# Kernel optimization log

Hardware: AMD Instinct MI355X
Metric: run time of the kernel (lower is better)

Reference implementation:

```python
import jax, jax.numpy as jnp
import numpy as np

S, B, I, H = 512, 64, 512, 512
KEEP = 0.75  # 1 - dropout_p, p = 0.25


def _mask(key, shape):
    # inverted-dropout mask, sampled once per sequence (variational dropout)
    return (jax.random.uniform(key, shape) < KEEP).astype(jnp.float32) / KEEP


def setup_inputs() -> dict:
    key = jax.random.key(0)
    ks = jax.random.split(key, 10)
    s_i0 = 1.0 / np.sqrt(I)
    s_i1 = 1.0 / np.sqrt(2 * H)
    s_h = 1.0 / np.sqrt(H)
    return {
        "x": jax.random.normal(ks[0], (S, B, I), jnp.float32),
        "W_ih_l0": jax.random.normal(ks[1], (2, 4 * H, I), jnp.float32) * s_i0,
        "W_ih_l1": jax.random.normal(ks[2], (2, 4 * H, 2 * H), jnp.float32) * s_i1,
        "W_hh": jax.random.normal(ks[3], (4, 4 * H, H), jnp.float32) * s_h,
        "b_ih": jax.random.normal(ks[4], (4, 4 * H), jnp.float32) * s_h,
        "b_hh": jax.random.normal(ks[5], (4, 4 * H), jnp.float32) * s_h,
        "mask_x0": _mask(ks[6], (2, B, I)),
        "mask_x1": _mask(ks[7], (2, B, 2 * H)),
        "mask_h": _mask(ks[8], (4, B, H)),
    }


def _run_cell(x, W_ih, W_hh, b_ih, b_hh, mx, mh, reverse):
    # x: [S, B, in]; returns out [S, B, H], (h_n, c_n) each [B, H]
    xs = x[::-1] if reverse else x
    # precompute input projections for all timesteps (one big GEMM)
    xp = jnp.einsum('sbi,gi->sbg', xs * mx, W_ih) + b_ih  # [S, B, 4H]
    h = W_hh.shape[1]
    h0 = jnp.zeros((x.shape[1], h), x.dtype)

    def step(carry, xp_t):
        hh, cc = carry
        gates = xp_t + (hh * mh) @ W_hh.T + b_hh  # variational hidden dropout
        gi, gf, gg, go = jnp.split(gates, 4, axis=-1)  # torch LSTMCell order i,f,g,o
        cc = jax.nn.sigmoid(gf) * cc + jax.nn.sigmoid(gi) * jnp.tanh(gg)
        hh = jax.nn.sigmoid(go) * jnp.tanh(cc)
        return (hh, cc), hh

    (hn, cn), out = jax.lax.scan(step, (h0, h0), xp)
    out = out[::-1] if reverse else out
    return out, hn, cn


def reference(x, W_ih_l0, W_ih_l1, W_hh, b_ih, b_hh, mask_x0, mask_x1, mask_h):
    W_ih = [W_ih_l0, W_ih_l1]
    mask_x = [mask_x0, mask_x1]
    inp = x
    h_list, c_list = [], []
    for layer in range(2):
        outs = []
        for d in range(2):  # 0: forward, 1: backward
            idx = 2 * layer + d
            o, hn, cn = _run_cell(inp, W_ih[layer][d], W_hh[idx], b_ih[idx],
                                  b_hh[idx], mask_x[layer][d], mask_h[idx],
                                  reverse=(d == 1))
            outs.append(o)
            h_list.append(hn)
            c_list.append(cn)
        inp = jnp.concatenate(outs, axis=-1)  # [S, B, 2H]
    return inp, jnp.stack(h_list, 0), jnp.stack(c_list, 0)
```

## Files before the change

### kernel.cpp

```cpp
#include <hip/hip_runtime.h>
#include <math.h>


typedef float f32x4 __attribute__((ext_vector_type(4)));

#define SLEN   512
#define HID    512
#define CHK    64
#define APAD   68
#define OUT_SEQ  (SLEN*64*2*HID)
#define STATE_SZ (4*64*HID)

__global__ __launch_bounds__(256) void init_ws(float* __restrict__ hmT,
                                               unsigned* __restrict__ bar) {
    const int b = blockIdx.x, t = threadIdx.x;
    if (b < 128) {
        *(f32x4*)(hmT + (b*256 + t)*4) = (f32x4){0.f, 0.f, 0.f, 0.f};
    } else {
        bar[(b - 128)*256 + t] = 0u;
    }
}

__device__ __forceinline__ void bar_arrive(unsigned* bar, int g) {
    __syncthreads();
    if (threadIdx.x == 0) {
        unsigned lo = __hip_atomic_fetch_add(bar + (g & 31)*16, 1u,
                          __ATOMIC_RELAXED, __HIP_MEMORY_SCOPE_AGENT);
        if (lo == 7u) {
            unsigned ro = __hip_atomic_fetch_add(bar + 512, 1u,
                              __ATOMIC_RELAXED, __HIP_MEMORY_SCOPE_AGENT);
            if (ro == 31u) {
                for (int i = 0; i < 32; ++i)
                    __hip_atomic_store(bar + i*16, 0u,
                        __ATOMIC_RELAXED, __HIP_MEMORY_SCOPE_AGENT);
                __hip_atomic_store(bar + 512, 0u,
                    __ATOMIC_RELAXED, __HIP_MEMORY_SCOPE_AGENT);
                asm volatile("s_waitcnt vmcnt(0)" ::: "memory");
                __hip_atomic_fetch_add(bar + 513, 1u,
                    __ATOMIC_RELAXED, __HIP_MEMORY_SCOPE_AGENT);
            }
        }
    }
}

__device__ __forceinline__ void bar_wait(unsigned* bar, unsigned s) {
    if (threadIdx.x == 0) {
        while (__hip_atomic_load(bar + 513, __ATOMIC_RELAXED,
                                 __HIP_MEMORY_SCOPE_AGENT) < s)
            __builtin_amdgcn_s_sleep(1);
    }
    __syncthreads();
}

template<int LAYER>
__global__ __launch_bounds__(256) void lstm_layer(
    const float* __restrict__ x,
    const float* __restrict__ Wih0,
    const float* __restrict__ Wih1,
    const float* __restrict__ Whh,
    const float* __restrict__ bih,
    const float* __restrict__ bhh,
    const float* __restrict__ mx0,
    const float* __restrict__ mx1,
    const float* __restrict__ mhm,
    float* __restrict__ out0,
    float* __restrict__ hmT,
    unsigned* __restrict__ barbase,
    float* __restrict__ dout)
{
    constexpr int Kin = LAYER ? 1024 : 512;
    constexpr int NCH = (Kin + HID)/CHK;
    constexpr int HCH = Kin/CHK;

    __shared__ __align__(16) float At[2][CHK*APAD];
    __shared__ __align__(16) float Wt[2][CHK*16];

    unsigned* bar  = barbase + LAYER*1024;

    const int g    = blockIdx.x;
    const int dir  = g >> 7;
    const int wg   = g & 127;
    const int cell = LAYER*2 + dir;
    const int u0   = wg*4;
    const int tid  = threadIdx.x;
    const int lane = tid & 63;
    const int wv   = tid >> 6;

    const int r0 = (lane & 15)*4;
    const int c0 = (lane >> 4)*4;

    const int sb = tid >> 2;
    const int ak = (tid & 3)*4;
    const int hr = tid >> 4;
    const int hb = (tid & 15)*4;
    const int wc   = tid >> 4;
    const int wko  = (tid & 15)*4;
    const int wkey = ((tid & 15) >> 1) & 3;
    const int wpc  = (((wc >> 2) ^ wkey) << 2) | (wc & 3);
    const int gcw  = (wc >> 2)*512 + u0 + (wc & 3);

    const int pbA = (((c0 >> 2) ^ ((wv*2    ) & 3)) << 2);
    const int pbB = (((c0 >> 2) ^ ((wv*2 + 1) & 3)) << 2);

    const int eb = tid & 63;
    const int eu = tid >> 6;
    const size_t sidx = ((size_t)(cell*64 + eb))*512 + u0 + eu;
    const float bsum[4] = {
        bih[cell*2048 + 0*512 + u0 + eu] + bhh[cell*2048 + 0*512 + u0 + eu],
        bih[cell*2048 + 1*512 + u0 + eu] + bhh[cell*2048 + 1*512 + u0 + eu],
        bih[cell*2048 + 2*512 + u0 + eu] + bhh[cell*2048 + 2*512 + u0 + eu],
        bih[cell*2048 + 3*512 + u0 + eu] + bhh[cell*2048 + 3*512 + u0 + eu] };
    const float mreg = mhm[sidx];
    float* const haddr0 = hmT + ((size_t)(cell*512 + u0 + eu))*64 + eb;
    float creg = 0.0f;

    for (int s = 0; s < SLEN; ++s) {
        const int t = dir ? (SLEN-1-s) : s;
        const float* hrd = hmT + (size_t)(s & 1)*STATE_SZ;
        float* const hwr = haddr0 + (size_t)((s + 1) & 1)*STATE_SZ;

        float acc[4][4];
#pragma unroll
        for (int i = 0; i < 4; ++i)
#pragma unroll
            for (int j = 0; j < 4; ++j) acc[i][j] = 0.0f;

        f32x4 va0, va1, va2, va3, vm0, vm1, vm2, vm3, w4;
        bool xpart = true;

        auto prefetch = [&](int ch) {
            const int k0 = ch*CHK;
            xpart = (k0 < Kin);
            if (xpart) {
                const float *asrc, *amsk, *wsrc;
                if (LAYER == 0) {
                    asrc = x   + ((size_t)(t*64   + sb))*512  + k0 + ak;
                    amsk = mx0 + ((size_t)(dir*64 + sb))*512  + k0 + ak;
                    wsrc = Wih0 + (size_t)dir*2048*512  + (size_t)gcw*512  + k0 + wko;
                } else {
                    asrc = out0 + ((size_t)(t*64   + sb))*1024 + k0 + ak;
                    amsk = mx1  + ((size_t)(dir*64 + sb))*1024 + k0 + ak;
                    wsrc = Wih1 + (size_t)dir*2048*1024 + (size_t)gcw*1024 + k0 + wko;
                }
                va0 = *(const f32x4*)(asrc);      vm0 = *(const f32x4*)(amsk);
                va1 = *(const f32x4*)(asrc + 16); vm1 = *(const f32x4*)(amsk + 16);
                va2 = *(const f32x4*)(asrc + 32); vm2 = *(const f32x4*)(amsk + 32);
                va3 = *(const f32x4*)(asrc + 48); vm3 = *(const f32x4*)(amsk + 48);
                w4  = *(const f32x4*)(wsrc);
            } else {
                const int kh = k0 - Kin;
                const float* hsrc = hrd + ((size_t)(cell*512 + kh + hr))*64 + hb;
                asm volatile("global_load_dwordx4 %0, %1, off sc0 sc1 nt"
                             : "=v"(va0) : "v"(hsrc)         : "memory");
                asm volatile("global_load_dwordx4 %0, %1, off sc0 sc1 nt"
                             : "=v"(va1) : "v"(hsrc + 16*64) : "memory");
                asm volatile("global_load_dwordx4 %0, %1, off sc0 sc1 nt"
                             : "=v"(va2) : "v"(hsrc + 32*64) : "memory");
                asm volatile("global_load_dwordx4 %0, %1, off sc0 sc1 nt"
                             : "=v"(va3) : "v"(hsrc + 48*64) : "memory");
                w4  = *(const f32x4*)(Whh + (size_t)cell*2048*512
                                           + (size_t)gcw*512 + kh + wko);
            }
        };

        auto writeb = [&](float* Ab, float* Wb) {
            if (xpart) {
#define WRQ(Q, V, M)  { \
                Ab[(ak + (Q)*16 + 0)*APAD + sb] = V.x*M.x; \
                Ab[(ak + (Q)*16 + 1)*APAD + sb] = V.y*M.y; \
                Ab[(ak + (Q)*16 + 2)*APAD + sb] = V.z*M.z; \
                Ab[(ak + (Q)*16 + 3)*APAD + sb] = V.w*M.w; }
                WRQ(0, va0, vm0) WRQ(1, va1, vm1) WRQ(2, va2, vm2) WRQ(3, va3, vm3)
#undef WRQ
            } else {
                asm volatile("s_waitcnt vmcnt(0)" ::: "memory");
                *(f32x4*)(Ab + (hr +  0)*APAD + hb) = va0;
                *(f32x4*)(Ab + (hr + 16)*APAD + hb) = va1;
                *(f32x4*)(Ab + (hr + 32)*APAD + hb) = va2;
                *(f32x4*)(Ab + (hr + 48)*APAD + hb) = va3;
            }
            Wb[(wko+0)*16 + wpc] = w4.x;
            Wb[(wko+1)*16 + wpc] = w4.y;
            Wb[(wko+2)*16 + wpc] = w4.z;
            Wb[(wko+3)*16 + wpc] = w4.w;
        };

        auto compute = [&](const float* Ab, const float* Wb) {
#pragma unroll
            for (int kk = 0; kk < 16; ++kk) {
                const int krow = wv*16 + kk;
                const f32x4 a = *(const f32x4*)(Ab + krow*APAD + r0);
                const f32x4 w = *(const f32x4*)(Wb + krow*16 + (kk < 8 ? pbA : pbB));
                acc[0][0] += a.x*w.x; acc[0][1] += a.x*w.y; acc[0][2] += a.x*w.z; acc[0][3] += a.x*w.w;
                acc[1][0] += a.y*w.x; acc[1][1] += a.y*w.y; acc[1][2] += a.y*w.z; acc[1][3] += a.y*w.w;
                acc[2][0] += a.z*w.x; acc[2][1] += a.z*w.y; acc[2][2] += a.z*w.z; acc[2][3] += a.z*w.w;
                acc[3][0] += a.w*w.x; acc[3][1] += a.w*w.y; acc[3][2] += a.w*w.z; acc[3][3] += a.w*w.w;
            }
        };

        prefetch(0);
        writeb(At[0], Wt[0]);
        for (int ch = 0; ch < NCH; ++ch) {
            __syncthreads();
            if (ch == HCH - 1 && s > 0)
                bar_wait(bar, (unsigned)s);
            const int p = ch & 1;
            if (ch + 1 < NCH) prefetch(ch + 1);
            compute(At[p], Wt[p]);
            if (ch + 1 < NCH) writeb(At[p^1], Wt[p^1]);
        }

        float* red = At[0];
#pragma unroll
        for (int j = 0; j < 4; ++j) {
            f32x4 v = {acc[0][j], acc[1][j], acc[2][j], acc[3][j]};
            *(f32x4*)(red + wv*1024 + (c0+j)*64 + r0) = v;
        }
        __syncthreads();

        {
            float gq[4];
#pragma unroll
            for (int q = 0; q < 4; ++q) {
                const int c = q*4 + eu;
                gq[q] = red[c*64 + eb] + red[1024 + c*64 + eb]
                      + red[2048 + c*64 + eb] + red[3072 + c*64 + eb] + bsum[q];
            }
            const float ig = 1.0f/(1.0f + expf(-gq[0]));
            const float fg = 1.0f/(1.0f + expf(-gq[1]));
            const float gg = tanhf(gq[2]);
            const float og = 1.0f/(1.0f + expf(-gq[3]));
            const float cnew = fg*creg + ig*gg;
            const float hnew = og*tanhf(cnew);
            creg = cnew;
            const float hm = hnew * mreg;
            asm volatile("global_store_dword %0, %1, off sc0 sc1 nt"
                         :: "v"(hwr), "v"(hm) : "memory");
            float* obase = LAYER ? dout : out0;
            obase[((size_t)(t*64 + eb))*1024 + dir*512 + u0 + eu] = hnew;
            if (s == SLEN-1) {
                dout[OUT_SEQ + sidx]            = hnew;
                dout[OUT_SEQ + STATE_SZ + sidx] = cnew;
            }
        }

        if (s + 1 < SLEN) bar_arrive(bar, g);
    }
}

extern "C" void kernel_launch(void* const* d_in, const int* in_sizes, int n_in,
                              void* d_out, int out_size, void* d_ws, size_t ws_size,
                              hipStream_t stream)
{
    const float* x    = (const float*)d_in[0];
    const float* Wih0 = (const float*)d_in[1];
    const float* Wih1 = (const float*)d_in[2];
    const float* Whh  = (const float*)d_in[3];
    const float* bih  = (const float*)d_in[4];
    const float* bhh  = (const float*)d_in[5];
    const float* mx0  = (const float*)d_in[6];
    const float* mx1  = (const float*)d_in[7];
    const float* mhm  = (const float*)d_in[8];

    float* out  = (float*)d_out;
    float* out0 = (float*)d_ws;
    float* hmT  = out0 + OUT_SEQ;
    unsigned* bar = (unsigned*)(hmT + 2*STATE_SZ);

    init_ws<<<136, 256, 0, stream>>>(hmT, bar);
    lstm_layer<0><<<256, 256, 0, stream>>>(x, Wih0, Wih1, Whh, bih, bhh,
                                           mx0, mx1, mhm, out0, hmT, bar, out);
    lstm_layer<1><<<256, 256, 0, stream>>>(x, Wih0, Wih1, Whh, bih, bhh,
                                           mx0, mx1, mhm, out0, hmT, bar, out);
}
```

Before: 29.07 ms.

## Pre-transpose weights to K-major layout and read them directly from global in 512-thread blocks

Adds a kernel that transposes the input and recurrent weights into one K-major buffer, so each block reads its weight columns as coalesced vector loads instead of staging them through shared memory. The recurrent kernel moves to 512 threads with 8 waves, each wave taking a half-K slice and computing 8 gate columns, and the two halves are combined with a cross-lane shuffle before the shared-memory reduction. This removes the weight LDS staging and its swizzle, and doubles the waves per block to hide latency. The cost is an extra transpose pass over all weights on every call and heavier per-step global/L2 weight traffic.

```diff
diff --git a/kernel.cpp b/kernel.cpp
--- a/kernel.cpp
+++ b/kernel.cpp
@@ -10,6 +10,7 @@
 #define APAD   68
 #define OUT_SEQ  (SLEN*64*2*HID)
 #define STATE_SZ (4*64*HID)
+#define WT_ROWS  5120
 
 __global__ __launch_bounds__(256) void init_ws(float* __restrict__ hmT,
                                                unsigned* __restrict__ bar) {
@@ -18,6 +19,50 @@
         *(f32x4*)(hmT + (b*256 + t)*4) = (f32x4){0.f, 0.f, 0.f, 0.f};
     } else {
         bar[(b - 128)*256 + t] = 0u;
+    }
+}
+
+__global__ __launch_bounds__(256) void transpose_w(
+    const float* __restrict__ Wih0,
+    const float* __restrict__ Wih1,
+    const float* __restrict__ Whh,
+    float* __restrict__ WT)
+{
+    int id = blockIdx.x;
+    int cell, rem;
+    if (id < 1024) { cell = id >> 9;            rem = id & 511; }
+    else { id -= 1024; cell = 2 + (id >= 768);  rem = id % 768; }
+    const int ktile = rem >> 5, gtile = rem & 31;
+    const int k0 = ktile*64, g0 = gtile*64;
+    const int Kin = (cell < 2) ? 512 : 1024;
+
+    const float* src; int ks; size_t srow;
+    if (k0 < Kin) {
+        src = (cell < 2) ? Wih0 + (size_t)cell*2048*512
+                         : Wih1 + (size_t)(cell-2)*2048*1024;
+        ks = k0; srow = Kin;
+    } else {
+        src = Whh + (size_t)cell*2048*512;
+        ks = k0 - Kin; srow = 512;
+    }
+
+    __shared__ float T[64][65];
+    const int tid = threadIdx.x;
+    {
+        const int i = tid >> 2, j0 = (tid & 3)*16;
+        const float* p = src + (size_t)(g0 + i)*srow + ks + j0;
+#pragma unroll
+        for (int q = 0; q < 4; ++q)
+            *(f32x4*)(&T[i][j0 + q*4]) = *(const f32x4*)(p + q*4);
+    }
+    __syncthreads();
+    {
+        const size_t rowOff = (cell == 0) ? 0 : (cell == 1) ? 1024
+                            : (cell == 2) ? 2048 : 3584;
+        const int jj0 = (tid >> 6)*16, ii = tid & 63;
+#pragma unroll
+        for (int jj = 0; jj < 16; ++jj)
+            WT[(rowOff + k0 + jj0 + jj)*2048 + g0 + ii] = T[ii][jj0 + jj];
     }
 }
 
@@ -53,11 +98,9 @@
 }
 
 template<int LAYER>
-__global__ __launch_bounds__(256) void lstm_layer(
+__global__ __launch_bounds__(512, 2) void lstm_layer(
     const float* __restrict__ x,
-    const float* __restrict__ Wih0,
-    const float* __restrict__ Wih1,
-    const float* __restrict__ Whh,
+    const float* __restrict__ WT,
     const float* __restrict__ bih,
     const float* __restrict__ bhh,
     const float* __restrict__ mx0,
@@ -73,9 +116,8 @@
     constexpr int HCH = Kin/CHK;
 
     __shared__ __align__(16) float At[2][CHK*APAD];
-    __shared__ __align__(16) float Wt[2][CHK*16];
-
-    unsigned* bar  = barbase + LAYER*1024;
+
+    unsigned* bar = barbase + LAYER*1024;
 
     const int g    = blockIdx.x;
     const int dir  = g >> 7;
@@ -86,32 +128,35 @@
     const int lane = tid & 63;
     const int wv   = tid >> 6;
 
-    const int r0 = (lane & 15)*4;
-    const int c0 = (lane >> 4)*4;
-
-    const int sb = tid >> 2;
-    const int ak = (tid & 3)*4;
-    const int hr = tid >> 4;
-    const int hb = (tid & 15)*4;
-    const int wc   = tid >> 4;
-    const int wko  = (tid & 15)*4;
-    const int wkey = ((tid & 15) >> 1) & 3;
-    const int wpc  = (((wc >> 2) ^ wkey) << 2) | (wc & 3);
-    const int gcw  = (wc >> 2)*512 + u0 + (wc & 3);
-
-    const int pbA = (((c0 >> 2) ^ ((wv*2    ) & 3)) << 2);
-    const int pbB = (((c0 >> 2) ^ ((wv*2 + 1) & 3)) << 2);
+    const int r0    = (lane & 15)*4;
+    const int cq    = (lane >> 4) & 1;
+    const int c0    = cq*8;
+    const int kbase = wv*8 + (lane >> 5)*4;
+    const int wcb   = cq*1024 + u0;
+    const size_t rowOff = LAYER ? (2048 + (size_t)dir*1536) : ((size_t)dir*1024);
+    const float* WTc = WT + rowOff*2048;
+
+    const int sb  = tid & 63;
+    const int aks = (tid >> 6)*8;
+    const int hkrow = tid >> 3;
+    const int hb    = (tid & 7)*8;
 
     const int eb = tid & 63;
     const int eu = tid >> 6;
-    const size_t sidx = ((size_t)(cell*64 + eb))*512 + u0 + eu;
-    const float bsum[4] = {
-        bih[cell*2048 + 0*512 + u0 + eu] + bhh[cell*2048 + 0*512 + u0 + eu],
-        bih[cell*2048 + 1*512 + u0 + eu] + bhh[cell*2048 + 1*512 + u0 + eu],
-        bih[cell*2048 + 2*512 + u0 + eu] + bhh[cell*2048 + 2*512 + u0 + eu],
-        bih[cell*2048 + 3*512 + u0 + eu] + bhh[cell*2048 + 3*512 + u0 + eu] };
-    const float mreg = mhm[sidx];
-    float* const haddr0 = hmT + ((size_t)(cell*512 + u0 + eu))*64 + eb;
+    float bsum[4] = {0.f, 0.f, 0.f, 0.f};
+    float mreg = 0.f;
+    float* haddr0 = nullptr;
+    size_t sidx = 0;
+    if (tid < 256) {
+#pragma unroll
+        for (int q = 0; q < 4; ++q) {
+            const int gc = cell*2048 + q*512 + u0 + eu;
+            bsum[q] = bih[gc] + bhh[gc];
+        }
+        sidx  = ((size_t)(cell*64 + eb))*512 + u0 + eu;
+        mreg  = mhm[sidx];
+        haddr0 = hmT + ((size_t)(cell*512 + u0 + eu))*64 + eb;
+    }
     float creg = 0.0f;
 
     for (int s = 0; s < SLEN; ++s) {
@@ -119,112 +164,108 @@
         const float* hrd = hmT + (size_t)(s & 1)*STATE_SZ;
         float* const hwr = haddr0 + (size_t)((s + 1) & 1)*STATE_SZ;
 
-        float acc[4][4];
+        float acc[4][8];
 #pragma unroll
         for (int i = 0; i < 4; ++i)
 #pragma unroll
-            for (int j = 0; j < 4; ++j) acc[i][j] = 0.0f;
-
-        f32x4 va0, va1, va2, va3, vm0, vm1, vm2, vm3, w4;
+            for (int j = 0; j < 8; ++j) acc[i][j] = 0.0f;
+
+        f32x4 va0, va1, vm0, vm1;
         bool xpart = true;
 
         auto prefetch = [&](int ch) {
             const int k0 = ch*CHK;
             xpart = (k0 < Kin);
             if (xpart) {
-                const float *asrc, *amsk, *wsrc;
+                const float *asrc, *amsk;
                 if (LAYER == 0) {
-                    asrc = x   + ((size_t)(t*64   + sb))*512  + k0 + ak;
-                    amsk = mx0 + ((size_t)(dir*64 + sb))*512  + k0 + ak;
-                    wsrc = Wih0 + (size_t)dir*2048*512  + (size_t)gcw*512  + k0 + wko;
+                    asrc = x   + ((size_t)(t*64   + sb))*512  + k0 + aks;
+                    amsk = mx0 + ((size_t)(dir*64 + sb))*512  + k0 + aks;
                 } else {
-                    asrc = out0 + ((size_t)(t*64   + sb))*1024 + k0 + ak;
-                    amsk = mx1  + ((size_t)(dir*64 + sb))*1024 + k0 + ak;
-                    wsrc = Wih1 + (size_t)dir*2048*1024 + (size_t)gcw*1024 + k0 + wko;
+                    asrc = out0 + ((size_t)(t*64   + sb))*1024 + k0 + aks;
+                    amsk = mx1  + ((size_t)(dir*64 + sb))*1024 + k0 + aks;
                 }
-                va0 = *(const f32x4*)(asrc);      vm0 = *(const f32x4*)(amsk);
-                va1 = *(const f32x4*)(asrc + 16); vm1 = *(const f32x4*)(amsk + 16);
-                va2 = *(const f32x4*)(asrc + 32); vm2 = *(const f32x4*)(amsk + 32);
-                va3 = *(const f32x4*)(asrc + 48); vm3 = *(const f32x4*)(amsk + 48);
-                w4  = *(const f32x4*)(wsrc);
+                va0 = *(const f32x4*)(asrc);     vm0 = *(const f32x4*)(amsk);
+                va1 = *(const f32x4*)(asrc + 4); vm1 = *(const f32x4*)(amsk + 4);
             } else {
                 const int kh = k0 - Kin;
-                const float* hsrc = hrd + ((size_t)(cell*512 + kh + hr))*64 + hb;
+                const float* hsrc = hrd + ((size_t)(cell*512 + kh + hkrow))*64 + hb;
                 asm volatile("global_load_dwordx4 %0, %1, off sc0 sc1 nt"
-                             : "=v"(va0) : "v"(hsrc)         : "memory");
+                             : "=v"(va0) : "v"(hsrc)     : "memory");
                 asm volatile("global_load_dwordx4 %0, %1, off sc0 sc1 nt"
-                             : "=v"(va1) : "v"(hsrc + 16*64) : "memory");
-                asm volatile("global_load_dwordx4 %0, %1, off sc0 sc1 nt"
-                             : "=v"(va2) : "v"(hsrc + 32*64) : "memory");
-                asm volatile("global_load_dwordx4 %0, %1, off sc0 sc1 nt"
-                             : "=v"(va3) : "v"(hsrc + 48*64) : "memory");
-                w4  = *(const f32x4*)(Whh + (size_t)cell*2048*512
-                                           + (size_t)gcw*512 + kh + wko);
+                             : "=v"(va1) : "v"(hsrc + 4) : "memory");
             }
         };
 
-        auto writeb = [&](float* Ab, float* Wb) {
+        auto writeb = [&](float* Ab) {
             if (xpart) {
-#define WRQ(Q, V, M)  { \
-                Ab[(ak + (Q)*16 + 0)*APAD + sb] = V.x*M.x; \
-                Ab[(ak + (Q)*16 + 1)*APAD + sb] = V.y*M.y; \
-                Ab[(ak + (Q)*16 + 2)*APAD + sb] = V.z*M.z; \
-                Ab[(ak + (Q)*16 + 3)*APAD + sb] = V.w*M.w; }
-                WRQ(0, va0, vm0) WRQ(1, va1, vm1) WRQ(2, va2, vm2) WRQ(3, va3, vm3)
-#undef WRQ
+                const f32x4 p0 = va0*vm0, p1 = va1*vm1;
+                float* col = Ab + aks*APAD + sb;
+                col[0*APAD] = p0.x; col[1*APAD] = p0.y;
+                col[2*APAD] = p0.z; col[3*APAD] = p0.w;
+                col[4*APAD] = p1.x; col[5*APAD] = p1.y;
+                col[6*APAD] = p1.z; col[7*APAD] = p1.w;
             } else {
                 asm volatile("s_waitcnt vmcnt(0)" ::: "memory");
-                *(f32x4*)(Ab + (hr +  0)*APAD + hb) = va0;
-                *(f32x4*)(Ab + (hr + 16)*APAD + hb) = va1;
-                *(f32x4*)(Ab + (hr + 32)*APAD + hb) = va2;
-                *(f32x4*)(Ab + (hr + 48)*APAD + hb) = va3;
-            }
-            Wb[(wko+0)*16 + wpc] = w4.x;
-            Wb[(wko+1)*16 + wpc] = w4.y;
-            Wb[(wko+2)*16 + wpc] = w4.z;
-            Wb[(wko+3)*16 + wpc] = w4.w;
+                *(f32x4*)(Ab + hkrow*APAD + hb)     = va0;
+                *(f32x4*)(Ab + hkrow*APAD + hb + 4) = va1;
+            }
         };
 
-        auto compute = [&](const float* Ab, const float* Wb) {
-#pragma unroll
-            for (int kk = 0; kk < 16; ++kk) {
-                const int krow = wv*16 + kk;
-                const f32x4 a = *(const f32x4*)(Ab + krow*APAD + r0);
-                const f32x4 w = *(const f32x4*)(Wb + krow*16 + (kk < 8 ? pbA : pbB));
-                acc[0][0] += a.x*w.x; acc[0][1] += a.x*w.y; acc[0][2] += a.x*w.z; acc[0][3] += a.x*w.w;
-                acc[1][0] += a.y*w.x; acc[1][1] += a.y*w.y; acc[1][2] += a.y*w.z; acc[1][3] += a.y*w.w;
-                acc[2][0] += a.z*w.x; acc[2][1] += a.z*w.y; acc[2][2] += a.z*w.z; acc[2][3] += a.z*w.w;
-                acc[3][0] += a.w*w.x; acc[3][1] += a.w*w.y; acc[3][2] += a.w*w.z; acc[3][3] += a.w*w.w;
+        auto compute = [&](const float* Ab, int k0) {
+#pragma unroll
+            for (int kk = 0; kk < 4; ++kk) {
+                const int krow = kbase + kk;
+                const f32x4 a  = *(const f32x4*)(Ab + krow*APAD + r0);
+                const float* wr = WTc + (size_t)(k0 + krow)*2048 + wcb;
+                const f32x4 w0 = *(const f32x4*)(wr);
+                const f32x4 w1 = *(const f32x4*)(wr + 512);
+#pragma unroll
+                for (int i = 0; i < 4; ++i) {
+                    acc[i][0] += a[i]*w0.x; acc[i][1] += a[i]*w0.y;
+                    acc[i][2] += a[i]*w0.z; acc[i][3] += a[i]*w0.w;
+                    acc[i][4] += a[i]*w1.x; acc[i][5] += a[i]*w1.y;
+                    acc[i][6] += a[i]*w1.z; acc[i][7] += a[i]*w1.w;
+                }
             }
         };
 
         prefetch(0);
-        writeb(At[0], Wt[0]);
+        writeb(At[0]);
         for (int ch = 0; ch < NCH; ++ch) {
             __syncthreads();
             if (ch == HCH - 1 && s > 0)
                 bar_wait(bar, (unsigned)s);
             const int p = ch & 1;
             if (ch + 1 < NCH) prefetch(ch + 1);
-            compute(At[p], Wt[p]);
-            if (ch + 1 < NCH) writeb(At[p^1], Wt[p^1]);
-        }
-
+            compute(At[p], ch*CHK);
+            if (ch + 1 < NCH) writeb(At[p^1]);
+        }
+
+#pragma unroll
+        for (int i = 0; i < 4; ++i)
+#pragma unroll
+            for (int j = 0; j < 8; ++j)
+                acc[i][j] += __shfl_xor(acc[i][j], 32);
         float* red = At[0];
-#pragma unroll
-        for (int j = 0; j < 4; ++j) {
-            f32x4 v = {acc[0][j], acc[1][j], acc[2][j], acc[3][j]};
-            *(f32x4*)(red + wv*1024 + (c0+j)*64 + r0) = v;
+        if (lane < 32) {
+#pragma unroll
+            for (int j = 0; j < 8; ++j) {
+                f32x4 v = {acc[0][j], acc[1][j], acc[2][j], acc[3][j]};
+                *(f32x4*)(red + wv*1024 + (c0 + j)*64 + r0) = v;
+            }
         }
         __syncthreads();
 
-        {
+        if (tid < 256) {
             float gq[4];
 #pragma unroll
             for (int q = 0; q < 4; ++q) {
                 const int c = q*4 + eu;
-                gq[q] = red[c*64 + eb] + red[1024 + c*64 + eb]
-                      + red[2048 + c*64 + eb] + red[3072 + c*64 + eb] + bsum[q];
+                float v = bsum[q];
+#pragma unroll
+                for (int w = 0; w < 8; ++w) v += red[w*1024 + c*64 + eb];
+                gq[q] = v;
             }
             const float ig = 1.0f/(1.0f + expf(-gq[0]));
             const float fg = 1.0f/(1.0f + expf(-gq[1]));
@@ -265,11 +306,13 @@
     float* out  = (float*)d_out;
     float* out0 = (float*)d_ws;
     float* hmT  = out0 + OUT_SEQ;
-    unsigned* bar = (unsigned*)(hmT + 2*STATE_SZ);
-
+    float* WT   = hmT + 2*STATE_SZ;
+    unsigned* bar = (unsigned*)(WT + (size_t)WT_ROWS*2048);
+
+    transpose_w<<<2560, 256, 0, stream>>>(Wih0, Wih1, Whh, WT);
     init_ws<<<136, 256, 0, stream>>>(hmT, bar);
-    lstm_layer<0><<<256, 256, 0, stream>>>(x, Wih0, Wih1, Whh, bih, bhh,
+    lstm_layer<0><<<256, 512, 0, stream>>>(x, WT, bih, bhh,
                                            mx0, mx1, mhm, out0, hmT, bar, out);
-    lstm_layer<1><<<256, 256, 0, stream>>>(x, Wih0, Wih1, Whh, bih, bhh,
+    lstm_layer<1><<<256, 512, 0, stream>>>(x, WT, bih, bhh,
                                            mx0, mx1, mhm, out0, hmT, bar, out);
 }
```

Result: slower. 42.71 ms (+46.9%).
